# Optimization experiments

Hardware: AMD Instinct MI355X
Metric: run time of the kernel (lower is better)

## Reference

```python
import jax, jax.numpy as jnp
import numpy as np

NUM_FRAMES = 8
NUM_CLASSES = 40
INNER_TH = 0.5
MIN_WH = 0.05
SUPPRESS = 1e9


def _xyxy_to_cxcywh(b):
    x1, y1, x2, y2 = b[..., 0], b[..., 1], b[..., 2], b[..., 3]
    return jnp.stack([(x1 + x2) * 0.5, (y1 + y2) * 0.5, x2 - x1, y2 - y1], -1)


def setup_inputs() -> dict:
    key = jax.random.key(0)
    k1, k2, k3, k4, k5 = jax.random.split(key, 5)
    B, N, T = 4, 20, NUM_FRAMES
    H = W = 160
    # valid xyxy boxes: centers in [0.1,0.9], wh in [0.02,0.3]
    c = jax.random.uniform(k1, (B, N, T, 2), minval=0.1, maxval=0.9)
    wh = jax.random.uniform(k2, (B, N, T, 2), minval=0.02, maxval=0.3)
    gt_boxes = jnp.concatenate([c - wh / 2, c + wh / 2], -1).astype(jnp.float32)
    gt_labels = jax.random.randint(k3, (B, N), 0, NUM_CLASSES)
    ids = jax.random.randint(k4, (B, N, T), 0, 100)
    drop = jax.random.bernoulli(k5, 0.1, (B, N, T))
    gt_ids = jnp.where(drop, -1, ids)  # -1 => instance absent in that frame
    ys, xs = jnp.meshgrid(jnp.arange(H), jnp.arange(W), indexing='ij')
    ref_points = jnp.stack([(xs.reshape(-1) + 0.5) / W, (ys.reshape(-1) + 0.5) / H], -1).astype(jnp.float32)
    spatial_shapes = jnp.array([H, W], dtype=jnp.int32)
    return dict(gt_labels=gt_labels, gt_boxes=gt_boxes, gt_ids=gt_ids,
                ref_points=ref_points, spatial_shapes=spatial_shapes)


def _match_frame(dist_t, ids_t, labels, valid):
    # dist_t [N,P], ids_t [N], labels [N], valid [N]; sequential suppression over n
    N, P = dist_t.shape
    arangeP = jnp.arange(P)
    arangeC = jnp.arange(NUM_CLASSES)

    def step(carry, n):
        d_all, ml, md, mi = carry
        d = d_all[n]                                   # [P]
        act = valid[n] & (ids_t[n] != -1)
        inner = d < INNER_TH
        # if no inner point, claim just the single closest point
        pos = jnp.where(inner.any(), inner, arangeP == jnp.argmin(d)) & act
        lab = labels[n]
        score = 1.0 - 2.0 * jnp.clip(d, 0.0, INNER_TH)
        ml = jnp.where(pos, lab, ml)
        md = jnp.where(pos[:, None] & (arangeC == lab)[None, :], score[:, None], md)
        mi = jnp.where(pos, ids_t[n], mi)
        d_all = jnp.where(pos[None, :], SUPPRESS, d_all)  # suppress claimed points for all gts
        return (d_all, ml, md, mi), None

    init = (dist_t,
            jnp.full((P,), -1, jnp.int32),
            jnp.zeros((P, NUM_CLASSES), dist_t.dtype),
            jnp.full((P,), -1, jnp.int32))
    (_, ml, md, mi), _ = jax.lax.scan(step, init, jnp.arange(N))
    return ml, md, mi


def reference(gt_labels, gt_boxes, gt_ids, ref_points, spatial_shapes):
    B, N, T, _ = gt_boxes.shape
    boxes_c = _xyxy_to_cxcywh(gt_boxes)                 # [B,N,T,4]
    area = (boxes_c[..., 2] * boxes_c[..., 3]).mean(-1)  # [B,N] mean area over frames
    order = jnp.argsort(area, axis=1)                   # process small instances first
    boxes_c = jnp.take_along_axis(boxes_c, order[:, :, None, None], axis=1)
    labels = jnp.take_along_axis(gt_labels.astype(jnp.int32), order, axis=1)
    ids = jnp.take_along_axis(gt_ids.astype(jnp.int32), order[:, :, None], axis=1)
    valid = (boxes_c[..., 2:] > 0.0).all(-1).any(-1) & (labels >= 0)  # [B,N]
    # normalized center distance: [B,N,T,P]
    diff = (boxes_c[..., None, :2] - ref_points[None, None, None, :, :]) / jnp.clip(boxes_c[..., None, 2:], MIN_WH)
    dist = jnp.sum(diff ** 2, -1)
    f = jax.vmap(jax.vmap(_match_frame, in_axes=(1, 1, None, None)), in_axes=(0, 0, 0, 0))
    ml, md, mi = f(dist, ids, labels, valid)            # [B,T,P], [B,T,P,C], [B,T,P]
    return ml, md, mi
```

## Files before the change

### kernel.cpp

```cpp
#include <hip/hip_runtime.h>

#define BB   4
#define NGT  20
#define TT   8
#define PP   25600
#define CC   40
#define TPB  1024
#define SUPP 1e9f
#define INNER_TH 0.5f
#define FILLB 224

#define PK_CLAIM  1u
#define PK_LAB_SH 1
#define PK_ID_SH  7
#define PK_MDV    (1u << 14)
#define PK_MDC_SH 15
#define PK_MDN_SH 21

__device__ inline unsigned long long shfl_down_u64(unsigned long long v, int off) {
    unsigned lo = (unsigned)v, hi = (unsigned)(v >> 32);
    lo = __shfl_down(lo, off, 64);
    hi = __shfl_down(hi, off, 64);
    return ((unsigned long long)hi << 32) | (unsigned long long)lo;
}

__device__ inline float4 make_geo(const float* __restrict__ gt_boxes, int b, int n, int t) {
    const float* bx = gt_boxes + ((size_t)(b * NGT + n) * TT + t) * 4;
    float x1 = bx[0], y1 = bx[1], x2 = bx[2], y2 = bx[3];
    float4 g;
    g.x = __fmul_rn(__fadd_rn(x1, x2), 0.5f);
    g.y = __fmul_rn(__fadd_rn(y1, y2), 0.5f);
    g.z = fmaxf(__fsub_rn(x2, x1), 0.05f);
    g.w = fmaxf(__fsub_rn(y2, y1), 0.05f);
    return g;
}

__device__ inline float point_dist(int px, int py, float4 g) {
    float rxv = __fdiv_rn((float)px + 0.5f, 160.0f);
    float ryv = __fdiv_rn((float)py + 0.5f, 160.0f);
    float dx = __fdiv_rn(__fsub_rn(g.x, rxv), g.z);
    float dy = __fdiv_rn(__fsub_rn(g.y, ryv), g.w);
    return __fadd_rn(__fmul_rn(dx, dx), __fmul_rn(dy, dy));
}

__global__ __launch_bounds__(TPB) void match_fill_kernel(
        const int*   __restrict__ gt_labels,
        const float* __restrict__ gt_boxes,
        const int*   __restrict__ gt_ids,
        unsigned* __restrict__ packs_g,
        uint4*    __restrict__ md4) {
    if (blockIdx.x >= BB * TT) {
        const int MD4 = BB * TT * PP * CC / 4;
        const int stride = FILLB * TPB;
        uint4 z = make_uint4(0u, 0u, 0u, 0u);
        for (int i = (blockIdx.x - BB * TT) * TPB + (int)threadIdx.x; i < MD4; i += stride)
            md4[i] = z;
        return;
    }

    int bt = blockIdx.x;
    int b  = bt >> 3;
    int t  = bt & 7;
    int tid  = threadIdx.x;
    int lane = tid & 63;
    int wav  = tid >> 6;

    __shared__ unsigned s_pack[PP];
    __shared__ unsigned s_mask[160 * 5];
    __shared__ float  s_dxx[NGT * 160];
    __shared__ float  s_dyy[NGT * 160];
    __shared__ float  s_area[NGT];
    __shared__ int    s_valid[NGT];
    __shared__ int    s_order[NGT];
    __shared__ int    s_any[NGT];
    __shared__ float4 s_geo[NGT];
    __shared__ int4   s_meta[NGT];
    __shared__ int    s_actlist[NGT];
    __shared__ int    s_actcnt;

    {
        uint4 z = make_uint4(0u, 0u, 0u, 0u);
        for (int i = tid; i < PP / 4; i += TPB) ((uint4*)s_pack)[i] = z;
    }
    if (tid < 160 * 5) s_mask[tid] = 0u;
    if (tid < NGT) {
        const float* bx = gt_boxes + (size_t)(b * NGT + tid) * TT * 4;
        float a[TT];
        int anyPos = 0;
        for (int f = 0; f < TT; f++) {
            float w = __fsub_rn(bx[f * 4 + 2], bx[f * 4 + 0]);
            float h = __fsub_rn(bx[f * 4 + 3], bx[f * 4 + 1]);
            a[f] = __fmul_rn(w, h);
            anyPos |= (w > 0.0f && h > 0.0f) ? 1 : 0;
        }
        float s = __fadd_rn(__fadd_rn(__fadd_rn(a[0], a[1]), __fadd_rn(a[2], a[3])),
                            __fadd_rn(__fadd_rn(a[4], a[5]), __fadd_rn(a[6], a[7])));
        s_area[tid]  = __fmul_rn(s, 0.125f);
        s_valid[tid] = (anyPos && gt_labels[b * NGT + tid] >= 0) ? 1 : 0;
        s_any[tid]   = 0;
    }
    __syncthreads();

    if (tid < NGT) {
        float an = s_area[tid];
        int r = 0;
        for (int m2 = 0; m2 < NGT; m2++) {
            float am = s_area[m2];
            r += (am < an || (am == an && m2 < tid)) ? 1 : 0;
        }
        s_order[r] = tid;
    }
    __syncthreads();

    if (tid < NGT) {
        int n   = s_order[tid];
        int src = b * NGT + n;
        s_geo[tid] = make_geo(gt_boxes, b, n, t);
        int id = gt_ids[src * TT + t];
        int4 mm;
        mm.x = gt_labels[src];
        mm.y = id;
        mm.z = (s_valid[n] && id != -1) ? 1 : 0;
        mm.w = n;
        s_meta[tid] = mm;
    }
    __syncthreads();
    if (tid == 0) {
        int c = 0;
        for (int k = 0; k < NGT; k++)
            if (s_meta[k].z) s_actlist[c++] = k;
        s_actcnt = c;
    }

    for (int i = tid; i < NGT * 320; i += TPB) {
        int slot = i / 320;
        int w    = i - slot * 320;
        float4 g = s_geo[slot];
        if (w < 160) {
            float rxv = __fdiv_rn((float)w + 0.5f, 160.0f);
            float dx  = __fdiv_rn(__fsub_rn(g.x, rxv), g.z);
            s_dxx[slot * 160 + w] = __fmul_rn(dx, dx);
        } else {
            int py = w - 160;
            float ryv = __fdiv_rn((float)py + 0.5f, 160.0f);
            float dy  = __fdiv_rn(__fsub_rn(g.y, ryv), g.w);
            s_dyy[slot * 160 + py] = __fmul_rn(dy, dy);
        }
    }
    __syncthreads();
    int actcnt = s_actcnt;

    for (int j = 0; j < actcnt; j++) {
        int slot = s_actlist[j];
        int4 m  = s_meta[slot];
        float4 g = s_geo[slot];
        const float* dxx = s_dxx + slot * 160;
        const float* dyy = s_dyy + slot * 160;

        float ex = __fmul_rn(g.z, 0.70711f);
        float ey = __fmul_rn(g.w, 0.70711f);
        int x0 = max(0,   (int)floorf((g.x - ex) * 160.0f - 0.5f) - 1);
        int x1 = min(159, (int)ceilf ((g.x + ex) * 160.0f - 0.5f) + 1);
        int y0 = max(0,   (int)floorf((g.y - ey) * 160.0f - 0.5f) - 1);
        int y1 = min(159, (int)ceilf ((g.y + ey) * 160.0f - 0.5f) + 1);
        int ax0 = x0 & ~31;

        unsigned base = PK_CLAIM | ((unsigned)m.x << PK_LAB_SH) |
                        ((unsigned)m.y << PK_ID_SH) | PK_MDV |
                        ((unsigned)m.x << PK_MDC_SH) |
                        ((unsigned)m.w << PK_MDN_SH);

        int wfound = 0;
        for (int y = y0 + wav; y <= y1; y += 16) {
            float dyyv = dyy[y];
            for (int ax = ax0; ax <= x1; ax += 64) {
                int x = ax + lane;
                int ok = 0;
                if (x < 160) {
                    unsigned mw = s_mask[y * 5 + (x >> 5)];
                    if (!((mw >> (x & 31)) & 1u)) {
                        float d = __fadd_rn(dxx[x], dyyv);
                        ok = (d < INNER_TH) ? 1 : 0;
                    }
                }
                unsigned long long ball = __ballot(ok);
                if (ok) s_pack[y * 160 + x] = base;
                if (ball) {
                    wfound = 1;
                    unsigned half = (unsigned)(ball >> (lane & 32));
                    if ((lane == 0 || lane == 32) && half)
                        s_mask[y * 5 + (ax >> 5) + (lane >> 5)] |= half;
                }
            }
        }
        if (lane == 0 && wfound) s_any[j] = 1;
        __syncthreads();

        if (!s_any[j]) {
            if (tid < 64) {
                unsigned long long key = ~0ULL;
                for (int y = tid; y < 160; y += 64) {
                    unsigned um[5];
#pragma unroll
                    for (int w = 0; w < 5; w++) um[w] = ~s_mask[y * 5 + w];
                    unsigned anyu = um[0] | um[1] | um[2] | um[3] | um[4];
                    if (!anyu) {
                        if (y == 0) {
                            unsigned long long kk =
                                ((unsigned long long)__float_as_uint(SUPP) << 32);
                            key = (kk < key) ? kk : key;
                        }
                        continue;
                    }
                    float dyyv = dyy[y];
                    int xs = (int)floorf(__fsub_rn(__fmul_rn(g.x, 160.0f), 0.5f));
                    xs = min(max(xs, -2), 161);
                    float bd = 2e9f;
                    int   bx = -1;
#pragma unroll
                    for (int k2 = 0; k2 < 2; k2++) {
                        int x = xs + k2;
                        if (x >= 0 && x <= 159 && ((um[x >> 5] >> (x & 31)) & 1u)) {
                            float d2 = __fadd_rn(dxx[x], dyyv);
                            if (d2 < bd || (d2 == bd && x < bx)) { bd = d2; bx = x; }
                        }
                    }
                    {
                        int xq = min(xs - 1, 159);
                        int xL = -1;
                        if (xq >= 0) {
                            int w = xq >> 5;
                            unsigned mm = um[w] & (0xffffffffu >> (31 - (xq & 31)));
                            while (true) {
                                if (mm) { xL = (w << 5) + (31 - __clz(mm)); break; }
                                if (--w < 0) break;
                                mm = um[w];
                            }
                        }
                        if (xL >= 0) {
                            float dL = __fadd_rn(dxx[xL], dyyv);
                            while (xL > 0) {
                                int xq2 = xL - 1;
                                int w = xq2 >> 5;
                                unsigned mm = um[w] & (0xffffffffu >> (31 - (xq2 & 31)));
                                int x2 = -1;
                                while (true) {
                                    if (mm) { x2 = (w << 5) + (31 - __clz(mm)); break; }
                                    if (--w < 0) break;
                                    mm = um[w];
                                }
                                if (x2 < 0) break;
                                if (__fadd_rn(dxx[x2], dyyv) != dL) break;
                                xL = x2;
                            }
                            if (dL < bd || (dL == bd && xL < bx)) { bd = dL; bx = xL; }
                        }
                    }
                    {
                        int xq = max(xs + 2, 0);
                        int xR = -1;
                        if (xq <= 159) {
                            int w = xq >> 5;
                            unsigned mm = um[w] & (0xffffffffu << (xq & 31));
                            while (true) {
                                if (mm) { xR = (w << 5) + (__ffs(mm) - 1); break; }
                                if (++w > 4) break;
                                mm = um[w];
                            }
                        }
                        if (xR >= 0) {
                            float dR = __fadd_rn(dxx[xR], dyyv);
                            if (dR < bd || (dR == bd && xR < bx)) { bd = dR; bx = xR; }
                        }
                    }
                    if (bx >= 0) {
                        int p = y * 160 + bx;
                        unsigned long long kk =
                            ((unsigned long long)__float_as_uint(bd) << 32) |
                            (unsigned long long)(unsigned)p;
                        key = (kk < key) ? kk : key;
                    }
                }
                unsigned long long v = key;
                for (int off = 32; off > 0; off >>= 1) {
                    unsigned long long o = shfl_down_u64(v, off);
                    v = (o < v) ? o : v;
                }
                if (tid == 0) {
                    float minv = __uint_as_float((unsigned)(v >> 32));
                    int minp = (int)(unsigned)(v & 0xffffffffu);
                    unsigned npk = PK_CLAIM | ((unsigned)m.x << PK_LAB_SH) |
                                   ((unsigned)m.y << PK_ID_SH);
                    if (minv < SUPP) {
                        s_pack[minp] = npk;
                    } else {
                        unsigned old = s_pack[minp];
                        unsigned mdbits = old & (PK_MDV | (63u << PK_MDC_SH) |
                                                 (31u << PK_MDN_SH));
                        if ((old & PK_MDV) &&
                            ((old >> PK_MDC_SH) & 63u) == (unsigned)m.x) mdbits = 0u;
                        s_pack[minp] = npk | mdbits;
                    }
                    s_mask[minp >> 5] |= 1u << (minp & 31);
                }
            }
            __syncthreads();
        }
    }

    __syncthreads();
    uint4* dst = (uint4*)(packs_g + (size_t)bt * PP);
    for (int i = tid; i < PP / 4; i += TPB) dst[i] = ((const uint4*)s_pack)[i];
}

__global__ __launch_bounds__(256) void scatter_kernel(
        const unsigned* __restrict__ packs,
        const float*    __restrict__ gt_boxes,
        float* __restrict__ out) {
    const int    ML = BB * TT * PP;
    const size_t MD = (size_t)BB * TT * PP * CC;
    int f = blockIdx.x * 256 + threadIdx.x;
    uint4 pk4 = ((const uint4*)packs)[f];

    float4 vml, vmi;
    vml.x = (pk4.x & PK_CLAIM) ? (float)((pk4.x >> PK_LAB_SH) & 63u) : -1.0f;
    vml.y = (pk4.y & PK_CLAIM) ? (float)((pk4.y >> PK_LAB_SH) & 63u) : -1.0f;
    vml.z = (pk4.z & PK_CLAIM) ? (float)((pk4.z >> PK_LAB_SH) & 63u) : -1.0f;
    vml.w = (pk4.w & PK_CLAIM) ? (float)((pk4.w >> PK_LAB_SH) & 63u) : -1.0f;
    vmi.x = (pk4.x & PK_CLAIM) ? (float)((pk4.x >> PK_ID_SH) & 127u) : -1.0f;
    vmi.y = (pk4.y & PK_CLAIM) ? (float)((pk4.y >> PK_ID_SH) & 127u) : -1.0f;
    vmi.z = (pk4.z & PK_CLAIM) ? (float)((pk4.z >> PK_ID_SH) & 127u) : -1.0f;
    vmi.w = (pk4.w & PK_CLAIM) ? (float)((pk4.w >> PK_ID_SH) & 127u) : -1.0f;
    ((float4*)out)[f] = vml;
    ((float4*)(out + ML + MD))[f] = vmi;

    int pt0 = f << 2;
#pragma unroll
    for (int k = 0; k < 4; k++) {
        unsigned pk = (k == 0) ? pk4.x : (k == 1) ? pk4.y : (k == 2) ? pk4.z : pk4.w;
        if (pk & PK_MDV) {
            int pt  = pt0 + k;
            int cls = (int)((pk >> PK_MDC_SH) & 63u);
            int n   = (int)((pk >> PK_MDN_SH) & 31u);
            int bt  = pt / PP;
            int p   = pt - bt * PP;
            int py  = p / 160;
            int px  = p - py * 160;
            float4 g = make_geo(gt_boxes, bt >> 3, n, bt & 7);
            float d  = point_dist(px, py, g);
            out[ML + (size_t)pt * CC + cls] = __fsub_rn(1.0f, __fmul_rn(2.0f, d));
        }
    }
}

extern "C" void kernel_launch(void* const* d_in, const int* in_sizes, int n_in,
                              void* d_out, int out_size, void* d_ws, size_t ws_size,
                              hipStream_t stream) {
    const int*   gt_labels = (const int*)d_in[0];
    const float* gt_boxes  = (const float*)d_in[1];
    const int*   gt_ids    = (const int*)d_in[2];

    unsigned* packs = (unsigned*)d_ws;
    float*    outf  = (float*)d_out;

    match_fill_kernel<<<BB * TT + FILLB, TPB, 0, stream>>>(
        gt_labels, gt_boxes, gt_ids, packs,
        (uint4*)(outf + BB * TT * PP));

    scatter_kernel<<<(BB * TT * PP / 4) / 256, 256, 0, stream>>>(packs, gt_boxes, outf);
}
```

Measured before the change: 173.7 us.

## Run per-frame matching in a single wavefront, replacing block barriers with wave barriers

The matching blocks now exit every wave except the first, so one 64-lane wavefront does all of the per-frame suppression work. Block-wide __syncthreads become wave barriers, and the active list is built with a ballot plus popcount. A snapshot of the mask rows is taken per gt so that in-loop mask updates do not affect other points in the same step. This removes barrier cost across the 20 sequential steps, but 16x fewer threads now handle the zero-fill, the distance tables, the inner-region scan and the copy-out, which could lengthen the serial critical path.

```diff
diff --git a/kernel.cpp b/kernel.cpp
--- a/kernel.cpp
+++ b/kernel.cpp
@@ -61,28 +61,27 @@
     int bt = blockIdx.x;
     int b  = bt >> 3;
     int t  = bt & 7;
-    int tid  = threadIdx.x;
-    int lane = tid & 63;
-    int wav  = tid >> 6;
+    int tid = threadIdx.x;
 
     __shared__ unsigned s_pack[PP];
     __shared__ unsigned s_mask[160 * 5];
+    __shared__ unsigned s_msnap[160 * 5];
     __shared__ float  s_dxx[NGT * 160];
     __shared__ float  s_dyy[NGT * 160];
     __shared__ float  s_area[NGT];
     __shared__ int    s_valid[NGT];
     __shared__ int    s_order[NGT];
-    __shared__ int    s_any[NGT];
     __shared__ float4 s_geo[NGT];
     __shared__ int4   s_meta[NGT];
     __shared__ int    s_actlist[NGT];
-    __shared__ int    s_actcnt;
+
+    if (tid >= 64) return;
 
     {
         uint4 z = make_uint4(0u, 0u, 0u, 0u);
-        for (int i = tid; i < PP / 4; i += TPB) ((uint4*)s_pack)[i] = z;
-    }
-    if (tid < 160 * 5) s_mask[tid] = 0u;
+        for (int i = tid; i < PP / 4; i += 64) ((uint4*)s_pack)[i] = z;
+        for (int i = tid; i < 200; i += 64) ((uint4*)s_mask)[i] = z;
+    }
     if (tid < NGT) {
         const float* bx = gt_boxes + (size_t)(b * NGT + tid) * TT * 4;
         float a[TT];
@@ -97,9 +96,8 @@
                             __fadd_rn(__fadd_rn(a[4], a[5]), __fadd_rn(a[6], a[7])));
         s_area[tid]  = __fmul_rn(s, 0.125f);
         s_valid[tid] = (anyPos && gt_labels[b * NGT + tid] >= 0) ? 1 : 0;
-        s_any[tid]   = 0;
-    }
-    __syncthreads();
+    }
+    __builtin_amdgcn_wave_barrier();
 
     if (tid < NGT) {
         float an = s_area[tid];
@@ -110,8 +108,9 @@
         }
         s_order[r] = tid;
     }
-    __syncthreads();
-
+    __builtin_amdgcn_wave_barrier();
+
+    int act = 0;
     if (tid < NGT) {
         int n   = s_order[tid];
         int src = b * NGT + n;
@@ -123,32 +122,29 @@
         mm.z = (s_valid[n] && id != -1) ? 1 : 0;
         mm.w = n;
         s_meta[tid] = mm;
-    }
-    __syncthreads();
-    if (tid == 0) {
-        int c = 0;
-        for (int k = 0; k < NGT; k++)
-            if (s_meta[k].z) s_actlist[c++] = k;
-        s_actcnt = c;
-    }
-
-    for (int i = tid; i < NGT * 320; i += TPB) {
-        int slot = i / 320;
-        int w    = i - slot * 320;
+        act = mm.z;
+    }
+    unsigned long long am = __ballot(act);
+    if (act) s_actlist[__popcll(am & ((1ull << tid) - 1ull))] = tid;
+    int actcnt = __popcll(am);
+    __builtin_amdgcn_wave_barrier();
+
+    for (int slot = 0; slot < NGT; slot++) {
         float4 g = s_geo[slot];
-        if (w < 160) {
-            float rxv = __fdiv_rn((float)w + 0.5f, 160.0f);
-            float dx  = __fdiv_rn(__fsub_rn(g.x, rxv), g.z);
-            s_dxx[slot * 160 + w] = __fmul_rn(dx, dx);
-        } else {
-            int py = w - 160;
-            float ryv = __fdiv_rn((float)py + 0.5f, 160.0f);
-            float dy  = __fdiv_rn(__fsub_rn(g.y, ryv), g.w);
-            s_dyy[slot * 160 + py] = __fmul_rn(dy, dy);
-        }
-    }
-    __syncthreads();
-    int actcnt = s_actcnt;
+        for (int w = tid; w < 320; w += 64) {
+            if (w < 160) {
+                float rxv = __fdiv_rn((float)w + 0.5f, 160.0f);
+                float dx  = __fdiv_rn(__fsub_rn(g.x, rxv), g.z);
+                s_dxx[slot * 160 + w] = __fmul_rn(dx, dx);
+            } else {
+                int py = w - 160;
+                float ryv = __fdiv_rn((float)py + 0.5f, 160.0f);
+                float dy  = __fdiv_rn(__fsub_rn(g.y, ryv), g.w);
+                s_dyy[slot * 160 + py] = __fmul_rn(dy, dy);
+            }
+        }
+    }
+    __builtin_amdgcn_wave_barrier();
 
     for (int j = 0; j < actcnt; j++) {
         int slot = s_actlist[j];
@@ -165,19 +161,27 @@
         int y1 = min(159, (int)ceilf ((g.y + ey) * 160.0f - 0.5f) + 1);
         int ax0 = x0 & ~31;
 
+        {
+            int nw = (y1 - y0 + 1) * 5;
+            int base5 = y0 * 5;
+            for (int i = tid; i < nw; i += 64)
+                s_msnap[base5 + i] = s_mask[base5 + i];
+        }
+        __builtin_amdgcn_wave_barrier();
+
         unsigned base = PK_CLAIM | ((unsigned)m.x << PK_LAB_SH) |
                         ((unsigned)m.y << PK_ID_SH) | PK_MDV |
                         ((unsigned)m.x << PK_MDC_SH) |
                         ((unsigned)m.w << PK_MDN_SH);
 
         int wfound = 0;
-        for (int y = y0 + wav; y <= y1; y += 16) {
+        for (int y = y0; y <= y1; y++) {
             float dyyv = dyy[y];
             for (int ax = ax0; ax <= x1; ax += 64) {
-                int x = ax + lane;
+                int x = ax + tid;
                 int ok = 0;
                 if (x < 160) {
-                    unsigned mw = s_mask[y * 5 + (x >> 5)];
+                    unsigned mw = s_msnap[y * 5 + (x >> 5)];
                     if (!((mw >> (x & 31)) & 1u)) {
                         float d = __fadd_rn(dxx[x], dyyv);
                         ok = (d < INNER_TH) ? 1 : 0;
@@ -187,130 +191,127 @@
                 if (ok) s_pack[y * 160 + x] = base;
                 if (ball) {
                     wfound = 1;
-                    unsigned half = (unsigned)(ball >> (lane & 32));
-                    if ((lane == 0 || lane == 32) && half)
-                        s_mask[y * 5 + (ax >> 5) + (lane >> 5)] |= half;
-                }
-            }
-        }
-        if (lane == 0 && wfound) s_any[j] = 1;
-        __syncthreads();
-
-        if (!s_any[j]) {
-            if (tid < 64) {
-                unsigned long long key = ~0ULL;
-                for (int y = tid; y < 160; y += 64) {
-                    unsigned um[5];
+                    unsigned half = (unsigned)(ball >> (tid & 32));
+                    if ((tid == 0 || tid == 32) && half)
+                        s_mask[y * 5 + (ax >> 5) + (tid >> 5)] |= half;
+                }
+            }
+        }
+        __builtin_amdgcn_wave_barrier();
+
+        if (!__any(wfound)) {
+            unsigned long long key = ~0ULL;
+            for (int y = tid; y < 160; y += 64) {
+                unsigned um[5];
 #pragma unroll
-                    for (int w = 0; w < 5; w++) um[w] = ~s_mask[y * 5 + w];
-                    unsigned anyu = um[0] | um[1] | um[2] | um[3] | um[4];
-                    if (!anyu) {
-                        if (y == 0) {
-                            unsigned long long kk =
-                                ((unsigned long long)__float_as_uint(SUPP) << 32);
-                            key = (kk < key) ? kk : key;
+                for (int w = 0; w < 5; w++) um[w] = ~s_mask[y * 5 + w];
+                unsigned anyu = um[0] | um[1] | um[2] | um[3] | um[4];
+                if (!anyu) {
+                    if (y == 0) {
+                        unsigned long long kk =
+                            ((unsigned long long)__float_as_uint(SUPP) << 32);
+                        key = (kk < key) ? kk : key;
+                    }
+                    continue;
+                }
+                float dyyv = dyy[y];
+                int xs = (int)floorf(__fsub_rn(__fmul_rn(g.x, 160.0f), 0.5f));
+                xs = min(max(xs, -2), 161);
+                float bd = 2e9f;
+                int   bx = -1;
+#pragma unroll
+                for (int k2 = 0; k2 < 2; k2++) {
+                    int x = xs + k2;
+                    if (x >= 0 && x <= 159 && ((um[x >> 5] >> (x & 31)) & 1u)) {
+                        float d2 = __fadd_rn(dxx[x], dyyv);
+                        if (d2 < bd || (d2 == bd && x < bx)) { bd = d2; bx = x; }
+                    }
+                }
+                {
+                    int xq = min(xs - 1, 159);
+                    int xL = -1;
+                    if (xq >= 0) {
+                        int w = xq >> 5;
+                        unsigned mm = um[w] & (0xffffffffu >> (31 - (xq & 31)));
+                        while (true) {
+                            if (mm) { xL = (w << 5) + (31 - __clz(mm)); break; }
+                            if (--w < 0) break;
+                            mm = um[w];
                         }
-                        continue;
-                    }
-                    float dyyv = dyy[y];
-                    int xs = (int)floorf(__fsub_rn(__fmul_rn(g.x, 160.0f), 0.5f));
-                    xs = min(max(xs, -2), 161);
-                    float bd = 2e9f;
-                    int   bx = -1;
-#pragma unroll
-                    for (int k2 = 0; k2 < 2; k2++) {
-                        int x = xs + k2;
-                        if (x >= 0 && x <= 159 && ((um[x >> 5] >> (x & 31)) & 1u)) {
-                            float d2 = __fadd_rn(dxx[x], dyyv);
-                            if (d2 < bd || (d2 == bd && x < bx)) { bd = d2; bx = x; }
-                        }
-                    }
-                    {
-                        int xq = min(xs - 1, 159);
-                        int xL = -1;
-                        if (xq >= 0) {
-                            int w = xq >> 5;
-                            unsigned mm = um[w] & (0xffffffffu >> (31 - (xq & 31)));
+                    }
+                    if (xL >= 0) {
+                        float dL = __fadd_rn(dxx[xL], dyyv);
+                        while (xL > 0) {
+                            int xq2 = xL - 1;
+                            int w = xq2 >> 5;
+                            unsigned mm = um[w] & (0xffffffffu >> (31 - (xq2 & 31)));
+                            int x2 = -1;
                             while (true) {
-                                if (mm) { xL = (w << 5) + (31 - __clz(mm)); break; }
+                                if (mm) { x2 = (w << 5) + (31 - __clz(mm)); break; }
                                 if (--w < 0) break;
                                 mm = um[w];
                             }
+                            if (x2 < 0) break;
+                            if (__fadd_rn(dxx[x2], dyyv) != dL) break;
+                            xL = x2;
                         }
-                        if (xL >= 0) {
-                            float dL = __fadd_rn(dxx[xL], dyyv);
-                            while (xL > 0) {
-                                int xq2 = xL - 1;
-                                int w = xq2 >> 5;
-                                unsigned mm = um[w] & (0xffffffffu >> (31 - (xq2 & 31)));
-                                int x2 = -1;
-                                while (true) {
-                                    if (mm) { x2 = (w << 5) + (31 - __clz(mm)); break; }
-                                    if (--w < 0) break;
-                                    mm = um[w];
-                                }
-                                if (x2 < 0) break;
-                                if (__fadd_rn(dxx[x2], dyyv) != dL) break;
-                                xL = x2;
-                            }
-                            if (dL < bd || (dL == bd && xL < bx)) { bd = dL; bx = xL; }
+                        if (dL < bd || (dL == bd && xL < bx)) { bd = dL; bx = xL; }
+                    }
+                }
+                {
+                    int xq = max(xs + 2, 0);
+                    int xR = -1;
+                    if (xq <= 159) {
+                        int w = xq >> 5;
+                        unsigned mm = um[w] & (0xffffffffu << (xq & 31));
+                        while (true) {
+                            if (mm) { xR = (w << 5) + (__ffs(mm) - 1); break; }
+                            if (++w > 4) break;
+                            mm = um[w];
                         }
                     }
-                    {
-                        int xq = max(xs + 2, 0);
-                        int xR = -1;
-                        if (xq <= 159) {
-                            int w = xq >> 5;
-                            unsigned mm = um[w] & (0xffffffffu << (xq & 31));
-                            while (true) {
-                                if (mm) { xR = (w << 5) + (__ffs(mm) - 1); break; }
-                                if (++w > 4) break;
-                                mm = um[w];
-                            }
-                        }
-                        if (xR >= 0) {
-                            float dR = __fadd_rn(dxx[xR], dyyv);
-                            if (dR < bd || (dR == bd && xR < bx)) { bd = dR; bx = xR; }
-                        }
-                    }
-                    if (bx >= 0) {
-                        int p = y * 160 + bx;
-                        unsigned long long kk =
-                            ((unsigned long long)__float_as_uint(bd) << 32) |
-                            (unsigned long long)(unsigned)p;
-                        key = (kk < key) ? kk : key;
-                    }
-                }
-                unsigned long long v = key;
-                for (int off = 32; off > 0; off >>= 1) {
-                    unsigned long long o = shfl_down_u64(v, off);
-                    v = (o < v) ? o : v;
-                }
-                if (tid == 0) {
-                    float minv = __uint_as_float((unsigned)(v >> 32));
-                    int minp = (int)(unsigned)(v & 0xffffffffu);
-                    unsigned npk = PK_CLAIM | ((unsigned)m.x << PK_LAB_SH) |
-                                   ((unsigned)m.y << PK_ID_SH);
-                    if (minv < SUPP) {
-                        s_pack[minp] = npk;
-                    } else {
-                        unsigned old = s_pack[minp];
-                        unsigned mdbits = old & (PK_MDV | (63u << PK_MDC_SH) |
-                                                 (31u << PK_MDN_SH));
-                        if ((old & PK_MDV) &&
-                            ((old >> PK_MDC_SH) & 63u) == (unsigned)m.x) mdbits = 0u;
-                        s_pack[minp] = npk | mdbits;
-                    }
-                    s_mask[minp >> 5] |= 1u << (minp & 31);
-                }
-            }
-            __syncthreads();
-        }
-    }
-
-    __syncthreads();
+                    if (xR >= 0) {
+                        float dR = __fadd_rn(dxx[xR], dyyv);
+                        if (dR < bd || (dR == bd && xR < bx)) { bd = dR; bx = xR; }
+                    }
+                }
+                if (bx >= 0) {
+                    int p = y * 160 + bx;
+                    unsigned long long kk =
+                        ((unsigned long long)__float_as_uint(bd) << 32) |
+                        (unsigned long long)(unsigned)p;
+                    key = (kk < key) ? kk : key;
+                }
+            }
+            unsigned long long v = key;
+            for (int off = 32; off > 0; off >>= 1) {
+                unsigned long long o = shfl_down_u64(v, off);
+                v = (o < v) ? o : v;
+            }
+            if (tid == 0) {
+                float minv = __uint_as_float((unsigned)(v >> 32));
+                int minp = (int)(unsigned)(v & 0xffffffffu);
+                unsigned npk = PK_CLAIM | ((unsigned)m.x << PK_LAB_SH) |
+                               ((unsigned)m.y << PK_ID_SH);
+                if (minv < SUPP) {
+                    s_pack[minp] = npk;
+                } else {
+                    unsigned old = s_pack[minp];
+                    unsigned mdbits = old & (PK_MDV | (63u << PK_MDC_SH) |
+                                             (31u << PK_MDN_SH));
+                    if ((old & PK_MDV) &&
+                        ((old >> PK_MDC_SH) & 63u) == (unsigned)m.x) mdbits = 0u;
+                    s_pack[minp] = npk | mdbits;
+                }
+                s_mask[minp >> 5] |= 1u << (minp & 31);
+            }
+            __builtin_amdgcn_wave_barrier();
+        }
+    }
+    __builtin_amdgcn_wave_barrier();
+
     uint4* dst = (uint4*)(packs_g + (size_t)bt * PP);
-    for (int i = tid; i < PP / 4; i += TPB) dst[i] = ((const uint4*)s_pack)[i];
+    for (int i = tid; i < PP / 4; i += 64) dst[i] = ((const uint4*)s_pack)[i];
 }
 
 __global__ __launch_bounds__(256) void scatter_kernel(
```

Measured after the change: 424.2 us. 2.44x slower.
